# Performance work log

Hardware: AMD Instinct MI355X
Metric: run time of the kernel (lower is better)

Reference implementation:

```python
import jax, jax.numpy as jnp
import numpy as np

K_NEIGHBORS = 5
EPS = 1e-12  # torch F.normalize eps


def _l2_normalize(x):
    n = jnp.linalg.norm(x, axis=-1, keepdims=True)
    return x / jnp.maximum(n, EPS)


def setup_inputs() -> dict:
    key = jax.random.key(0)
    k1, k2, k3, k4 = jax.random.split(key, 4)
    B, D = 256, 512
    N, A = 50000, 8
    return {
        "z_flowed": jax.random.normal(k1, (B, D), dtype=jnp.float32),
        "target_attrs": jax.random.randint(k2, (B, A), 0, 3, dtype=jnp.int32),
        "train_embeddings": jax.random.normal(k3, (N, D), dtype=jnp.float32),
        "train_attributes": jax.random.randint(k4, (N, A), 0, 3, dtype=jnp.int32),
    }


def reference(z_flowed, target_attrs, train_embeddings, train_attributes):
    B = z_flowed.shape[0]
    A = target_attrs.shape[1]
    z_norm = _l2_normalize(z_flowed)          # [B, D]
    train_norm = _l2_normalize(train_embeddings)  # [N, D]

    # batched attribute match: [B, N] count of matching attributes
    match_score = (train_attributes[None, :, :] == target_attrs[:, None, :]).sum(-1)
    mask = (match_score >= (A - 1)).astype(z_norm.dtype)  # [B, N]

    # cosine similarities for all samples in one GEMM: [B, N]
    sims = jnp.einsum('nd,bd->bn', train_norm, z_norm)
    masked_sim = sims * mask

    top_k_values, _ = jax.lax.top_k(masked_sim, K_NEIGHBORS)  # [B, K]
    per_sample_loss = (1.0 - top_k_values).mean(-1)           # [B]

    # samples with fewer than k matching neighbors are skipped in the sum
    valid = (mask.sum(-1) >= K_NEIGHBORS).astype(per_sample_loss.dtype)
    return (per_sample_loss * valid).sum() / B
```

## Files before the change

### kernel.cpp

```cpp
#include <hip/hip_runtime.h>
#include <math.h>


constexpr int D = 512;
constexpr int A = 8;
constexpr int K_NEI = 5;
constexpr int SLOTS = 512;
constexpr int CSTRIDE = 16;
constexpr int PAIR_CAP = 65536;
constexpr int LDS_PAIR_CAP = 1024;
constexpr int DOT_BLOCKS = 2048;

__device__ __forceinline__ float wave_reduce_add(float v) {
    #pragma unroll
    for (int m = 1; m < 64; m <<= 1) v += __shfl_xor(v, m, 64);
    return v;
}

__global__ __launch_bounds__(64) void prep_kernel(
    const float* __restrict__ z, const int* __restrict__ tattr,
    float* __restrict__ z_norm, unsigned* __restrict__ tpacked,
    int* __restrict__ counters, int* __restrict__ npairs,
    float* __restrict__ out)
{
    const int b = blockIdx.x;
    const int lane = threadIdx.x;
    const float4* zrow = (const float4*)(z + (size_t)b * D);
    float4 v0 = zrow[lane * 2 + 0];
    float4 v1 = zrow[lane * 2 + 1];
    float ss = v0.x*v0.x + v0.y*v0.y + v0.z*v0.z + v0.w*v0.w
             + v1.x*v1.x + v1.y*v1.y + v1.z*v1.z + v1.w*v1.w;
    ss = wave_reduce_add(ss);
    const float scale = 1.0f / fmaxf(sqrtf(ss), 1e-12f);
    v0.x *= scale; v0.y *= scale; v0.z *= scale; v0.w *= scale;
    v1.x *= scale; v1.y *= scale; v1.z *= scale; v1.w *= scale;
    float4* orow = (float4*)(z_norm + (size_t)b * D);
    orow[lane * 2 + 0] = v0;
    orow[lane * 2 + 1] = v1;
    if (lane == 0) {
        unsigned p = 0;
        #pragma unroll
        for (int a = 0; a < A; a++)
            p |= ((unsigned)tattr[b * A + a] & 0xFu) << (4 * a);
        tpacked[b] = p;
        counters[b * CSTRIDE] = 0;
        if (b == 0) { *npairs = 0; out[0] = 0.0f; }
    }
}

__global__ __launch_bounds__(256) void match_kernel(
    const int* __restrict__ trattr, const unsigned* __restrict__ tpacked,
    unsigned* __restrict__ pairs, int* __restrict__ npairs, int N)
{
    __shared__ unsigned s_tp[256];
    __shared__ unsigned s_pairs[LDS_PAIR_CAP];
    __shared__ int s_cnt, s_base;

    const int tid = threadIdx.x;
    const int n = blockIdx.x * 256 + tid;
    s_tp[tid] = tpacked[tid];
    if (tid == 0) s_cnt = 0;
    __syncthreads();

    if (n < N) {
        const int4* a4 = (const int4*)(trattr + (size_t)n * A);
        const int4 x = a4[0], y = a4[1];
        const unsigned p =
             ((unsigned)x.x & 0xFu)        | (((unsigned)x.y & 0xFu) << 4)
           | (((unsigned)x.z & 0xFu) << 8)  | (((unsigned)x.w & 0xFu) << 12)
           | (((unsigned)y.x & 0xFu) << 16) | (((unsigned)y.y & 0xFu) << 20)
           | (((unsigned)y.z & 0xFu) << 24) | (((unsigned)y.w & 0xFu) << 28);

        const uint4* tp4 = (const uint4*)s_tp;
        #pragma unroll 4
        for (int bq = 0; bq < 64; bq++) {
            const uint4 t = tp4[bq];
            #pragma unroll
            for (int j = 0; j < 4; j++) {
                const unsigned tv = (j == 0) ? t.x : (j == 1) ? t.y : (j == 2) ? t.z : t.w;
                const unsigned yv = p ^ tv;
                const unsigned nzhi = ((((yv & 0x77777777u) + 0x77777777u) | yv) & 0x88888888u);
                if (__popc(nzhi) <= 1) {
                    const int idx = atomicAdd(&s_cnt, 1);
                    if (idx < LDS_PAIR_CAP)
                        s_pairs[idx] = ((unsigned)n << 8) | (unsigned)(bq * 4 + j);
                }
            }
        }
    }
    __syncthreads();
    const int cnt = min(s_cnt, LDS_PAIR_CAP);
    if (tid == 0) s_base = atomicAdd(npairs, cnt);
    __syncthreads();
    const int base = s_base;
    for (int i = tid; i < cnt; i += 256)
        if (base + i < PAIR_CAP) pairs[base + i] = s_pairs[i];
}

__global__ __launch_bounds__(256) void dot_kernel(
    const float* __restrict__ train, const float* __restrict__ z_norm,
    const unsigned* __restrict__ pairs, const int* __restrict__ npairs,
    int* __restrict__ counters, float* __restrict__ simbuf)
{
    const int lane = threadIdx.x & 63;
    const int w = blockIdx.x * 4 + (threadIdx.x >> 6);
    const int nwaves = DOT_BLOCKS * 4;
    const int np = min(*npairs, PAIR_CAP);

    const int niter = (np - w + nwaves - 1) / nwaves;
    if (niter <= 0) return;
    const int myidx = w + lane * nwaves;
    const unsigned mypr = (myidx < np && lane < niter) ? pairs[myidx] : 0u;

    unsigned pr = __shfl(mypr, 0, 64);
    const float4* row4 = (const float4*)(train  + (size_t)(pr >> 8)   * D);
    const float4* zr4  = (const float4*)(z_norm + (size_t)(pr & 255u) * D);
    float4 r0 = row4[lane * 2 + 0];
    float4 r1 = row4[lane * 2 + 1];
    float4 z0 = zr4[lane * 2 + 0];
    float4 z1 = zr4[lane * 2 + 1];

    for (int t = 0; t < niter; t++) {
        float4 nr0, nr1, nz0, nz1;
        const bool more = (t + 1 < niter);
        if (more) {
            const unsigned npr = __shfl(mypr, t + 1, 64);
            const float4* nrow4 = (const float4*)(train  + (size_t)(npr >> 8)   * D);
            const float4* nzr4  = (const float4*)(z_norm + (size_t)(npr & 255u) * D);
            nr0 = nrow4[lane * 2 + 0];
            nr1 = nrow4[lane * 2 + 1];
            nz0 = nzr4[lane * 2 + 0];
            nz1 = nzr4[lane * 2 + 1];
        }

        float ss = r0.x*r0.x + r0.y*r0.y + r0.z*r0.z + r0.w*r0.w
                 + r1.x*r1.x + r1.y*r1.y + r1.z*r1.z + r1.w*r1.w;
        float dd = r0.x*z0.x + r0.y*z0.y + r0.z*z0.z + r0.w*z0.w
                 + r1.x*z1.x + r1.y*z1.y + r1.z*z1.z + r1.w*z1.w;
        #pragma unroll
        for (int m = 1; m < 64; m <<= 1) {
            ss += __shfl_xor(ss, m, 64);
            dd += __shfl_xor(dd, m, 64);
        }
        if (lane == 0) {
            const int b = (int)(pr & 255u);
            const float sim = dd / fmaxf(sqrtf(ss), 1e-12f);
            const int idx = atomicAdd(&counters[b * CSTRIDE], 1);
            if (idx < SLOTS) simbuf[(size_t)b * SLOTS + idx] = sim;
        }

        if (more) {
            pr = __shfl(mypr, t + 1, 64);
            r0 = nr0; r1 = nr1; z0 = nz0; z1 = nz1;
        }
    }
}

__global__ __launch_bounds__(64) void topk_kernel(
    const int* __restrict__ counters, const float* __restrict__ simbuf,
    float* __restrict__ out, int Bt)
{
    const int b = blockIdx.x;
    const int lane = threadIdx.x;
    const int cnt = counters[b * CSTRIDE];
    const int m = min(cnt, SLOTS);
    const float* buf = simbuf + (size_t)b * SLOTS;

    float v[8];
    #pragma unroll
    for (int k = 0; k < 8; k++) {
        const int i = lane + k * 64;
        v[k] = (i < m) ? buf[i] : -1e30f;
    }

    float s = 0.0f;
    #pragma unroll
    for (int r = 0; r < K_NEI; r++) {
        float best = v[0];
        #pragma unroll
        for (int k = 1; k < 8; k++) best = fmaxf(best, v[k]);
        float M = best;
        #pragma unroll
        for (int mm = 1; mm < 64; mm <<= 1) M = fmaxf(M, __shfl_xor(M, mm, 64));
        s += fmaxf(M, 0.0f);
        const unsigned long long bal = __ballot(best == M);
        const int first = __ffsll(bal) - 1;
        if (lane == first) {
            if      (v[0] == M) v[0] = -1e30f;
            else if (v[1] == M) v[1] = -1e30f;
            else if (v[2] == M) v[2] = -1e30f;
            else if (v[3] == M) v[3] = -1e30f;
            else if (v[4] == M) v[4] = -1e30f;
            else if (v[5] == M) v[5] = -1e30f;
            else if (v[6] == M) v[6] = -1e30f;
            else                v[7] = -1e30f;
        }
    }

    if (lane == 0) {
        const float contrib = (cnt >= K_NEI) ? (1.0f - s * (1.0f / K_NEI)) : 0.0f;
        atomicAdd(out, contrib / (float)Bt);
    }
}

extern "C" void kernel_launch(void* const* d_in, const int* in_sizes, int n_in,
                              void* d_out, int out_size, void* d_ws, size_t ws_size,
                              hipStream_t stream)
{
    const float* z      = (const float*)d_in[0];
    const int*   tattr  = (const int*)d_in[1];
    const float* train  = (const float*)d_in[2];
    const int*   trattr = (const int*)d_in[3];
    float* out = (float*)d_out;

    const int B = in_sizes[0] / D;
    const int N = in_sizes[2] / D;

    char* ws = (char*)d_ws;
    float*    z_norm   = (float*)ws;    ws += (size_t)B * D * sizeof(float);
    unsigned* tpacked  = (unsigned*)ws; ws += (size_t)B * sizeof(unsigned);
    int*      counters = (int*)ws;      ws += (size_t)B * CSTRIDE * sizeof(int);
    float*    simbuf   = (float*)ws;    ws += (size_t)B * SLOTS * sizeof(float);
    int*      npairs   = (int*)ws;      ws += 64;
    unsigned* pairs    = (unsigned*)ws;

    prep_kernel<<<B, 64, 0, stream>>>(z, tattr, z_norm, tpacked, counters, npairs, out);
    match_kernel<<<(N + 255) / 256, 256, 0, stream>>>(trattr, tpacked, pairs, npairs, N);
    dot_kernel<<<DOT_BLOCKS, 256, 0, stream>>>(train, z_norm, pairs, npairs, counters, simbuf);
    topk_kernel<<<B, 64, 0, stream>>>(counters, simbuf, out, B);
}
```

Baseline: 177.5 us.

## Replace global atomics with fixed per-block pair slots and deterministic reductions

Match kernel now writes pairs into fixed per-block slots of capacity 256 with a per-block count, dropping the global atomic compaction and LDS staging. The dot kernel walks all slots (sentinel for empty ones) and writes similarities directly by slot, removing per-pair atomic counters. Top-k now scans the entire slot array per query block (256 blocks each reading all slots) and a final kernel sums contributions instead of atomics. This trades atomics and nondeterminism for many wasted empty-slot iterations and repeated full scans in top-k.

After: 254.2 us. 1.43x slower.

```diff
diff --git a/kernel.cpp b/kernel.cpp
--- a/kernel.cpp
+++ b/kernel.cpp
@@ -5,11 +5,9 @@
 constexpr int D = 512;
 constexpr int A = 8;
 constexpr int K_NEI = 5;
-constexpr int SLOTS = 512;
-constexpr int CSTRIDE = 16;
-constexpr int PAIR_CAP = 65536;
-constexpr int LDS_PAIR_CAP = 1024;
+constexpr int CAP = 256;
 constexpr int DOT_BLOCKS = 2048;
+constexpr unsigned SENT = 0xFFFFFFFFu;
 
 __device__ __forceinline__ float wave_reduce_add(float v) {
     #pragma unroll
@@ -19,9 +17,7 @@
 
 __global__ __launch_bounds__(64) void prep_kernel(
     const float* __restrict__ z, const int* __restrict__ tattr,
-    float* __restrict__ z_norm, unsigned* __restrict__ tpacked,
-    int* __restrict__ counters, int* __restrict__ npairs,
-    float* __restrict__ out)
+    float* __restrict__ z_norm, unsigned* __restrict__ tpacked)
 {
     const int b = blockIdx.x;
     const int lane = threadIdx.x;
@@ -43,18 +39,15 @@
         for (int a = 0; a < A; a++)
             p |= ((unsigned)tattr[b * A + a] & 0xFu) << (4 * a);
         tpacked[b] = p;
-        counters[b * CSTRIDE] = 0;
-        if (b == 0) { *npairs = 0; out[0] = 0.0f; }
     }
 }
 
 __global__ __launch_bounds__(256) void match_kernel(
     const int* __restrict__ trattr, const unsigned* __restrict__ tpacked,
-    unsigned* __restrict__ pairs, int* __restrict__ npairs, int N)
+    unsigned* __restrict__ pairs, int* __restrict__ cnt, int N)
 {
     __shared__ unsigned s_tp[256];
-    __shared__ unsigned s_pairs[LDS_PAIR_CAP];
-    __shared__ int s_cnt, s_base;
+    __shared__ int s_cnt;
 
     const int tid = threadIdx.x;
     const int n = blockIdx.x * 256 + tid;
@@ -82,125 +75,150 @@
                 const unsigned nzhi = ((((yv & 0x77777777u) + 0x77777777u) | yv) & 0x88888888u);
                 if (__popc(nzhi) <= 1) {
                     const int idx = atomicAdd(&s_cnt, 1);
-                    if (idx < LDS_PAIR_CAP)
-                        s_pairs[idx] = ((unsigned)n << 8) | (unsigned)(bq * 4 + j);
+                    if (idx < CAP)
+                        pairs[blockIdx.x * CAP + idx] =
+                            ((unsigned)n << 8) | (unsigned)(bq * 4 + j);
                 }
             }
         }
     }
     __syncthreads();
-    const int cnt = min(s_cnt, LDS_PAIR_CAP);
-    if (tid == 0) s_base = atomicAdd(npairs, cnt);
-    __syncthreads();
-    const int base = s_base;
-    for (int i = tid; i < cnt; i += 256)
-        if (base + i < PAIR_CAP) pairs[base + i] = s_pairs[i];
+    if (tid == 0) cnt[blockIdx.x] = min(s_cnt, CAP);
 }
 
 __global__ __launch_bounds__(256) void dot_kernel(
     const float* __restrict__ train, const float* __restrict__ z_norm,
-    const unsigned* __restrict__ pairs, const int* __restrict__ npairs,
-    int* __restrict__ counters, float* __restrict__ simbuf)
+    const unsigned* __restrict__ pairs, const int* __restrict__ cnt,
+    float* __restrict__ sims, int TOT)
 {
     const int lane = threadIdx.x & 63;
     const int w = blockIdx.x * 4 + (threadIdx.x >> 6);
     const int nwaves = DOT_BLOCKS * 4;
-    const int np = min(*npairs, PAIR_CAP);
-
-    const int niter = (np - w + nwaves - 1) / nwaves;
+    const int niter = (TOT - w + nwaves - 1) / nwaves;
     if (niter <= 0) return;
-    const int myidx = w + lane * nwaves;
-    const unsigned mypr = (myidx < np && lane < niter) ? pairs[myidx] : 0u;
+
+    unsigned mypr = SENT;
+    if (lane < niter) {
+        const int slot = w + lane * nwaves;
+        if ((slot & (CAP - 1)) < cnt[slot >> 8]) mypr = pairs[slot];
+    }
 
     unsigned pr = __shfl(mypr, 0, 64);
-    const float4* row4 = (const float4*)(train  + (size_t)(pr >> 8)   * D);
-    const float4* zr4  = (const float4*)(z_norm + (size_t)(pr & 255u) * D);
-    float4 r0 = row4[lane * 2 + 0];
-    float4 r1 = row4[lane * 2 + 1];
-    float4 z0 = zr4[lane * 2 + 0];
-    float4 z1 = zr4[lane * 2 + 1];
+    float4 r0 = {0,0,0,0}, r1 = {0,0,0,0}, z0 = {0,0,0,0}, z1 = {0,0,0,0};
+    if (pr != SENT) {
+        const float4* row4 = (const float4*)(train  + (size_t)(pr >> 8)   * D);
+        const float4* zr4  = (const float4*)(z_norm + (size_t)(pr & 255u) * D);
+        r0 = row4[lane * 2 + 0]; r1 = row4[lane * 2 + 1];
+        z0 = zr4[lane * 2 + 0];  z1 = zr4[lane * 2 + 1];
+    }
 
     for (int t = 0; t < niter; t++) {
-        float4 nr0, nr1, nz0, nz1;
+        const int slot = w + t * nwaves;
         const bool more = (t + 1 < niter);
+        unsigned npr = SENT;
+        float4 nr0 = {0,0,0,0}, nr1 = {0,0,0,0}, nz0 = {0,0,0,0}, nz1 = {0,0,0,0};
         if (more) {
-            const unsigned npr = __shfl(mypr, t + 1, 64);
-            const float4* nrow4 = (const float4*)(train  + (size_t)(npr >> 8)   * D);
-            const float4* nzr4  = (const float4*)(z_norm + (size_t)(npr & 255u) * D);
-            nr0 = nrow4[lane * 2 + 0];
-            nr1 = nrow4[lane * 2 + 1];
-            nz0 = nzr4[lane * 2 + 0];
-            nz1 = nzr4[lane * 2 + 1];
-        }
-
-        float ss = r0.x*r0.x + r0.y*r0.y + r0.z*r0.z + r0.w*r0.w
-                 + r1.x*r1.x + r1.y*r1.y + r1.z*r1.z + r1.w*r1.w;
-        float dd = r0.x*z0.x + r0.y*z0.y + r0.z*z0.z + r0.w*z0.w
-                 + r1.x*z1.x + r1.y*z1.y + r1.z*z1.z + r1.w*z1.w;
+            npr = __shfl(mypr, t + 1, 64);
+            if (npr != SENT) {
+                const float4* nrow4 = (const float4*)(train  + (size_t)(npr >> 8)   * D);
+                const float4* nzr4  = (const float4*)(z_norm + (size_t)(npr & 255u) * D);
+                nr0 = nrow4[lane * 2 + 0]; nr1 = nrow4[lane * 2 + 1];
+                nz0 = nzr4[lane * 2 + 0];  nz1 = nzr4[lane * 2 + 1];
+            }
+        }
+
+        if (pr != SENT) {
+            float ss = r0.x*r0.x + r0.y*r0.y + r0.z*r0.z + r0.w*r0.w
+                     + r1.x*r1.x + r1.y*r1.y + r1.z*r1.z + r1.w*r1.w;
+            float dd = r0.x*z0.x + r0.y*z0.y + r0.z*z0.z + r0.w*z0.w
+                     + r1.x*z1.x + r1.y*z1.y + r1.z*z1.z + r1.w*z1.w;
+            #pragma unroll
+            for (int m = 1; m < 64; m <<= 1) {
+                ss += __shfl_xor(ss, m, 64);
+                dd += __shfl_xor(dd, m, 64);
+            }
+            if (lane == 0) sims[slot] = dd / fmaxf(sqrtf(ss), 1e-12f);
+        } else {
+            if (lane == 0) sims[slot] = -1e30f;
+        }
+
+        pr = npr; r0 = nr0; r1 = nr1; z0 = nz0; z1 = nz1;
+    }
+}
+
+__global__ __launch_bounds__(256) void topk_kernel(
+    const unsigned* __restrict__ pairs, const float* __restrict__ sims,
+    float* __restrict__ contrib, int TOT, int Bt)
+{
+    const int b = blockIdx.x;
+    const int tid = threadIdx.x;
+    const int lane = tid & 63;
+    const int wv = tid >> 6;
+
+    float top[K_NEI];
+    #pragma unroll
+    for (int k = 0; k < K_NEI; k++) top[k] = -1e30f;
+    int mc = 0;
+
+    for (int s = tid; s < TOT; s += 256) {
+        const unsigned pr = pairs[s];
+        const float v = sims[s];
+        if ((pr & 255u) == (unsigned)b && v > -1e29f) {
+            mc++;
+            if (v > top[K_NEI - 1]) {
+                top[K_NEI - 1] = v;
+                #pragma unroll
+                for (int k = K_NEI - 1; k > 0; k--)
+                    if (top[k] > top[k - 1]) { float tt = top[k]; top[k] = top[k - 1]; top[k - 1] = tt; }
+            }
+        }
+    }
+
+    __shared__ int s_mc[4];
+    __shared__ float s_wmax[4];
+
+    int mcw = mc;
+    #pragma unroll
+    for (int m = 1; m < 64; m <<= 1) mcw += __shfl_xor(mcw, m, 64);
+    if (lane == 0) s_mc[wv] = mcw;
+    __syncthreads();
+    const int cntb = s_mc[0] + s_mc[1] + s_mc[2] + s_mc[3];
+
+    float ssum = 0.0f;
+    #pragma unroll
+    for (int r = 0; r < K_NEI; r++) {
+        const float cand = top[0];
+        float Mw = cand;
         #pragma unroll
-        for (int m = 1; m < 64; m <<= 1) {
-            ss += __shfl_xor(ss, m, 64);
-            dd += __shfl_xor(dd, m, 64);
-        }
-        if (lane == 0) {
-            const int b = (int)(pr & 255u);
-            const float sim = dd / fmaxf(sqrtf(ss), 1e-12f);
-            const int idx = atomicAdd(&counters[b * CSTRIDE], 1);
-            if (idx < SLOTS) simbuf[(size_t)b * SLOTS + idx] = sim;
-        }
-
-        if (more) {
-            pr = __shfl(mypr, t + 1, 64);
-            r0 = nr0; r1 = nr1; z0 = nz0; z1 = nz1;
-        }
-    }
-}
-
-__global__ __launch_bounds__(64) void topk_kernel(
-    const int* __restrict__ counters, const float* __restrict__ simbuf,
-    float* __restrict__ out, int Bt)
-{
-    const int b = blockIdx.x;
-    const int lane = threadIdx.x;
-    const int cnt = counters[b * CSTRIDE];
-    const int m = min(cnt, SLOTS);
-    const float* buf = simbuf + (size_t)b * SLOTS;
-
-    float v[8];
-    #pragma unroll
-    for (int k = 0; k < 8; k++) {
-        const int i = lane + k * 64;
-        v[k] = (i < m) ? buf[i] : -1e30f;
-    }
-
+        for (int m = 1; m < 64; m <<= 1) Mw = fmaxf(Mw, __shfl_xor(Mw, m, 64));
+        if (lane == 0) s_wmax[wv] = Mw;
+        __syncthreads();
+        const float M = fmaxf(fmaxf(s_wmax[0], s_wmax[1]), fmaxf(s_wmax[2], s_wmax[3]));
+        const int winw = (s_wmax[0] == M) ? 0 : (s_wmax[1] == M) ? 1 : (s_wmax[2] == M) ? 2 : 3;
+        if (wv == winw) {
+            const unsigned long long bal = __ballot(cand == M);
+            const int first = __ffsll(bal) - 1;
+            if (lane == first) {
+                #pragma unroll
+                for (int k = 0; k < K_NEI - 1; k++) top[k] = top[k + 1];
+                top[K_NEI - 1] = -1e30f;
+            }
+        }
+        ssum += fmaxf(M, 0.0f);
+        __syncthreads();
+    }
+
+    if (tid == 0)
+        contrib[b] = (cntb >= K_NEI) ? (1.0f - ssum * (1.0f / K_NEI)) / (float)Bt : 0.0f;
+}
+
+__global__ __launch_bounds__(64) void final_kernel(
+    const float* __restrict__ contrib, float* __restrict__ out, int Bt)
+{
     float s = 0.0f;
-    #pragma unroll
-    for (int r = 0; r < K_NEI; r++) {
-        float best = v[0];
-        #pragma unroll
-        for (int k = 1; k < 8; k++) best = fmaxf(best, v[k]);
-        float M = best;
-        #pragma unroll
-        for (int mm = 1; mm < 64; mm <<= 1) M = fmaxf(M, __shfl_xor(M, mm, 64));
-        s += fmaxf(M, 0.0f);
-        const unsigned long long bal = __ballot(best == M);
-        const int first = __ffsll(bal) - 1;
-        if (lane == first) {
-            if      (v[0] == M) v[0] = -1e30f;
-            else if (v[1] == M) v[1] = -1e30f;
-            else if (v[2] == M) v[2] = -1e30f;
-            else if (v[3] == M) v[3] = -1e30f;
-            else if (v[4] == M) v[4] = -1e30f;
-            else if (v[5] == M) v[5] = -1e30f;
-            else if (v[6] == M) v[6] = -1e30f;
-            else                v[7] = -1e30f;
-        }
-    }
-
-    if (lane == 0) {
-        const float contrib = (cnt >= K_NEI) ? (1.0f - s * (1.0f / K_NEI)) : 0.0f;
-        atomicAdd(out, contrib / (float)Bt);
-    }
+    for (int i = threadIdx.x; i < Bt; i += 64) s += contrib[i];
+    s = wave_reduce_add(s);
+    if (threadIdx.x == 0) out[0] = s;
 }
 
 extern "C" void kernel_launch(void* const* d_in, const int* in_sizes, int n_in,
@@ -215,17 +233,20 @@
 
     const int B = in_sizes[0] / D;
     const int N = in_sizes[2] / D;
+    const int NBLK = (N + 255) / 256;
+    const int TOT = NBLK * CAP;
 
     char* ws = (char*)d_ws;
-    float*    z_norm   = (float*)ws;    ws += (size_t)B * D * sizeof(float);
-    unsigned* tpacked  = (unsigned*)ws; ws += (size_t)B * sizeof(unsigned);
-    int*      counters = (int*)ws;      ws += (size_t)B * CSTRIDE * sizeof(int);
-    float*    simbuf   = (float*)ws;    ws += (size_t)B * SLOTS * sizeof(float);
-    int*      npairs   = (int*)ws;      ws += 64;
-    unsigned* pairs    = (unsigned*)ws;
-
-    prep_kernel<<<B, 64, 0, stream>>>(z, tattr, z_norm, tpacked, counters, npairs, out);
-    match_kernel<<<(N + 255) / 256, 256, 0, stream>>>(trattr, tpacked, pairs, npairs, N);
-    dot_kernel<<<DOT_BLOCKS, 256, 0, stream>>>(train, z_norm, pairs, npairs, counters, simbuf);
-    topk_kernel<<<B, 64, 0, stream>>>(counters, simbuf, out, B);
-}
+    float*    z_norm  = (float*)ws;    ws += (size_t)B * D * sizeof(float);
+    unsigned* tpacked = (unsigned*)ws; ws += (size_t)B * sizeof(unsigned);
+    int*      cnt     = (int*)ws;      ws += (size_t)NBLK * sizeof(int) + 48;
+    unsigned* pairs   = (unsigned*)ws; ws += (size_t)TOT * sizeof(unsigned);
+    float*    sims    = (float*)ws;    ws += (size_t)TOT * sizeof(float);
+    float*    contrib = (float*)ws;
+
+    prep_kernel<<<B, 64, 0, stream>>>(z, tattr, z_norm, tpacked);
+    match_kernel<<<NBLK, 256, 0, stream>>>(trattr, tpacked, pairs, cnt, N);
+    dot_kernel<<<DOT_BLOCKS, 256, 0, stream>>>(train, z_norm, pairs, cnt, sims, TOT);
+    topk_kernel<<<B, 256, 0, stream>>>(pairs, sims, contrib, TOT, B);
+    final_kernel<<<1, 64, 0, stream>>>(contrib, out, B);
+}
```
